# Performance work log

Hardware: AMD Instinct MI355X
Metric: run time of the kernel (lower is better)

The kernel has to match this reference:

```python
import jax, jax.numpy as jnp
import numpy as np

FX, FY, CX, CY = 48.0, 48.0, 48.0, 36.0
H, W = int(2 * CY), int(2 * CX)  # 72, 96
N = H * W  # 6912


def _yz1_grid():
    # K layout as in source: [[cx, fx, 0], [cy, 0, fy], [1, 0, 0]]
    K = np.array([[CX, FX, 0.0], [CY, 0.0, FY], [1.0, 0.0, 0.0]], dtype=np.float64)
    invK = np.linalg.inv(K).astype(np.float32)
    u = np.arange(W, dtype=np.float32)
    v = np.arange(H, dtype=np.float32)
    uu = np.tile(u, H)              # row-major flatten of (H, W) u-grid
    vv = np.repeat(v, W)
    uv1 = np.stack([uu, vv, np.ones_like(uu)], axis=0)  # (3, N)
    return jnp.asarray(invK @ uv1)  # (3, N)


def _kern_mat(p1, p2, dist_coef):
    # p1: (B,3,N1), p2: (B,3,N2) -> exp(-||p1_i - p2_j|| * coef): (B,N1,N2)
    sq1 = jnp.sum(p1 * p1, axis=1)                      # (B,N1)
    sq2 = jnp.sum(p2 * p2, axis=1)                      # (B,N2)
    cross = jnp.einsum('bcn,bcm->bnm', p1, p2)          # (B,N1,N2)
    d2 = jnp.maximum(sq1[:, :, None] + sq2[:, None, :] - 2.0 * cross, 0.0)
    return jnp.exp(-jnp.sqrt(d2) * dist_coef)


def _gramian_feat(f1, f2):
    # norm_mode=1, kernalize=False, L2_norm=True path of gramian()
    B, C = f1.shape[0], f1.shape[1]
    ff1 = f1.reshape(B, C, -1)                          # (B,C,N1)
    ff2 = f2.reshape(B, C, -1)
    n1 = jnp.linalg.norm(ff1, axis=1)                   # (B,N1)
    n2 = jnp.linalg.norm(ff2, axis=1)
    fea_norm_sum = jnp.sum(n1) + jnp.sum(n2)
    ff1 = ff1 / n1[:, None, :]
    ff2 = ff2 / n2[:, None, :]
    gram = jnp.einsum('bcn,bcm->bnm', ff1, ff2)         # (B,N1,N2)
    return gram, fea_norm_sum


def reference(feature1, feature2, depth1, depth2, pose1_2, pose1_2_noise, img1, img2):
    B = depth1.shape[0]
    yz1 = _yz1_grid()                                    # (3,N)
    xyz1 = yz1[None] * depth1.reshape(B, 1, -1)          # (B,3,N)
    xyz2 = yz1[None] * depth2.reshape(B, 1, -1)

    ones = jnp.ones((B, 1, xyz2.shape[2]), dtype=xyz2.dtype)
    xyz2_homo = jnp.concatenate([xyz2, ones], axis=1)    # (B,4,N)
    xyz2_trans = jnp.matmul(pose1_2, xyz2_homo)[:, 0:3, :]

    gram_feat, fea_norm_sum = _gramian_feat(feature1, feature2)
    pcl_diff_exp = _kern_mat(xyz1, xyz2_trans, 0.1)

    fea_norm_sum = fea_norm_sum * 100.0                  # L2_norm & diff_mode

    pose_noisy = jnp.matmul(pose1_2, pose1_2_noise)      # (B,4,4)
    xyz2_trans_noisy = jnp.matmul(pose_noisy, xyz2_homo)[:, 0:3, :]
    pcl_diff_exp_noisy = _kern_mat(xyz1, xyz2_trans_noisy, 0.1)

    inner_neg = -jnp.sum((pcl_diff_exp - pcl_diff_exp_noisy) * gram_feat)
    final_loss = inner_neg                               # sparse_mode=False
    return final_loss, inner_neg, fea_norm_sum


def setup_inputs() -> dict:
    key = jax.random.key(0)
    ks = jax.random.split(key, 8)
    B, C = 1, 16
    feature1 = jax.random.normal(ks[0], (B, C, H, W), dtype=jnp.float32)
    feature2 = jax.random.normal(ks[1], (B, C, H, W), dtype=jnp.float32)
    depth1 = jax.random.uniform(ks[2], (B, 1, H, W), dtype=jnp.float32, minval=0.5, maxval=5.0)
    depth2 = jax.random.uniform(ks[3], (B, 1, H, W), dtype=jnp.float32, minval=0.5, maxval=5.0)
    # pose near identity (rigid-ish transform with small perturbation)
    eye = jnp.eye(4, dtype=jnp.float32)
    dp = 0.05 * jax.random.normal(ks[4], (4, 4), dtype=jnp.float32)
    pose1_2 = (eye + dp.at[3].set(0.0))[None]           # (1,4,4), keep last row [0,0,0,1]
    dn = 0.05 * jax.random.normal(ks[5], (4, 4), dtype=jnp.float32)
    pose1_2_noise = eye + dn.at[3].set(0.0)
    img1 = jax.random.uniform(ks[6], (B, 3, H, W), dtype=jnp.float32)
    img2 = jax.random.uniform(ks[7], (B, 3, H, W), dtype=jnp.float32)
    return {"feature1": feature1, "feature2": feature2, "depth1": depth1,
            "depth2": depth2, "pose1_2": pose1_2, "pose1_2_noise": pose1_2_noise,
            "img1": img1, "img2": img2}
```

## Files before the change

kernel.cpp:

```cpp
#include <hip/hip_runtime.h>
#include <math.h>

#define NPIX 6912
#define IMW  96
#define NJC  64
#define JLEN (NPIX / NJC)

#define OFF_PACK1 0
#define OFF_PACK2 (OFF_PACK1 + NPIX * 4)
#define OFF_F1N   (OFF_PACK2 + NPIX * 8)
#define OFF_F2N   (OFF_F1N + NPIX * 16)

#if __has_builtin(__builtin_amdgcn_exp2f)
#define EXP2F(x) __builtin_amdgcn_exp2f(x)
#else
#define EXP2F(x) exp2f(x)
#endif
#if __has_builtin(__builtin_amdgcn_sqrtf)
#define SQRTF(x) __builtin_amdgcn_sqrtf(x)
#else
#define SQRTF(x) sqrtf(x)
#endif
#define NEG_COEF_LOG2E (-0.14426950408889634f)

__device__ __forceinline__ float blk_reduce256(float v) {
  __shared__ float sm[4];
#pragma unroll
  for (int o = 32; o > 0; o >>= 1) v += __shfl_down(v, o, 64);
  const int lane = threadIdx.x & 63;
  const int wv = threadIdx.x >> 6;
  if (lane == 0) sm[wv] = v;
  __syncthreads();
  return (sm[0] + sm[1]) + (sm[2] + sm[3]);
}

__global__ __launch_bounds__(256) void k_pre(
    const float* __restrict__ f1, const float* __restrict__ f2,
    const float* __restrict__ dep1, const float* __restrict__ dep2,
    const float* __restrict__ pose, const float* __restrict__ noise,
    float* __restrict__ ws, float* __restrict__ out) {
  __shared__ float sPose[24];
  const int t = threadIdx.x;
  if (t < 12) {
    sPose[t] = pose[t];
  } else if (t < 24) {
    const int u = t - 12, r = u >> 2, c = u & 3;
    float s = 0.f;
#pragma unroll
    for (int k = 0; k < 4; ++k) s = fmaf(pose[r * 4 + k], noise[k * 4 + c], s);
    sPose[t] = s;
  }
  __syncthreads();

  const int i = blockIdx.x * 256 + t;
  const int vi = i / IMW;
  const int ui = i - vi * IMW;
  const float inv48 = (float)(1.0 / 48.0);
  const float p1c = fmaf((float)ui, inv48, -1.0f);
  const float p2c = fmaf((float)vi, inv48, -0.75f);

  const float d1 = dep1[i];
  const float x0 = d1, x1 = d1 * p1c, x2 = d1 * p2c;
  const float sq1 = fmaf(x2, x2, fmaf(x1, x1, x0 * x0));
  *(float4*)(ws + OFF_PACK1 + (size_t)i * 4) = make_float4(x0, x1, x2, sq1);

  const float d2 = dep2[i];
  const float w0 = d2, w1 = d2 * p1c, w2 = d2 * p2c;
  const float* P  = sPose;
  const float* Pn = sPose + 12;
  const float y0 = fmaf(P[0], w0, fmaf(P[1], w1, fmaf(P[2],  w2, P[3])));
  const float y1 = fmaf(P[4], w0, fmaf(P[5], w1, fmaf(P[6],  w2, P[7])));
  const float y2 = fmaf(P[8], w0, fmaf(P[9], w1, fmaf(P[10], w2, P[11])));
  const float sq2 = fmaf(y2, y2, fmaf(y1, y1, y0 * y0));
  const float z0 = fmaf(Pn[0], w0, fmaf(Pn[1], w1, fmaf(Pn[2],  w2, Pn[3])));
  const float z1 = fmaf(Pn[4], w0, fmaf(Pn[5], w1, fmaf(Pn[6],  w2, Pn[7])));
  const float z2 = fmaf(Pn[8], w0, fmaf(Pn[9], w1, fmaf(Pn[10], w2, Pn[11])));
  const float sq2n = fmaf(z2, z2, fmaf(z1, z1, z0 * z0));
  *(float4*)(ws + OFF_PACK2 + (size_t)i * 8)     = make_float4(y0, y1, y2, sq2);
  *(float4*)(ws + OFF_PACK2 + (size_t)i * 8 + 4) = make_float4(z0, z1, z2, sq2n);

  float a[16], b[16];
  float sa = 0.f, sb = 0.f;
#pragma unroll
  for (int c = 0; c < 16; ++c) {
    a[c] = f1[c * NPIX + i]; sa = fmaf(a[c], a[c], sa);
    b[c] = f2[c * NPIX + i]; sb = fmaf(b[c], b[c], sb);
  }
  const float na = sqrtf(sa), nb = sqrtf(sb);
#pragma unroll
  for (int c = 0; c < 16; ++c) { a[c] = a[c] / na; b[c] = b[c] / nb; }
#pragma unroll
  for (int c = 0; c < 16; c += 4) {
    *(float4*)(ws + OFF_F1N + (size_t)i * 16 + c) = make_float4(a[c], a[c+1], a[c+2], a[c+3]);
    *(float4*)(ws + OFF_F2N + (size_t)i * 16 + c) = make_float4(b[c], b[c+1], b[c+2], b[c+3]);
  }
  const float part = blk_reduce256(na + nb);
  if (t == 0) atomicAdd(out + 2, 100.0f * part);
}

__global__ __launch_bounds__(256) void k_main(const float* __restrict__ ws,
                                              float* __restrict__ out) {
  __shared__ float4 sF[JLEN * 4];
  __shared__ float4 sP[JLEN * 2];

  const int j0 = blockIdx.y * JLEN;
  const float4* gF = (const float4*)(ws + OFF_F2N)   + (size_t)j0 * 4;
  const float4* gP = (const float4*)(ws + OFF_PACK2) + (size_t)j0 * 2;
  for (int tt = threadIdx.x; tt < JLEN * 4; tt += 256) sF[tt] = gF[tt];
  for (int tt = threadIdx.x; tt < JLEN * 2; tt += 256) sP[tt] = gP[tt];

  const int i = blockIdx.x * 256 + threadIdx.x;
  const float4 pk = *(const float4*)(ws + OFF_PACK1 + (size_t)i * 4);
  const float x0 = pk.x, x1 = pk.y, x2 = pk.z, sq1 = pk.w;
  float f1r[16];
#pragma unroll
  for (int c = 0; c < 16; c += 4) {
    const float4 tq = *(const float4*)(ws + OFF_F1N + (size_t)i * 16 + c);
    f1r[c] = tq.x; f1r[c+1] = tq.y; f1r[c+2] = tq.z; f1r[c+3] = tq.w;
  }
  __syncthreads();

  float acc0 = 0.f, acc1 = 0.f;
#pragma unroll 2
  for (int jj = 0; jj < JLEN; ++jj) {
    const float4 fa = sF[jj * 4 + 0];
    const float4 fb = sF[jj * 4 + 1];
    const float4 fc = sF[jj * 4 + 2];
    const float4 fd = sF[jj * 4 + 3];
    const float4 q  = sP[jj * 2 + 0];
    const float4 r  = sP[jj * 2 + 1];

    float g0 = fmaf(f1r[12], fd.x, fmaf(f1r[8],  fc.x, fmaf(f1r[4], fb.x, f1r[0] * fa.x)));
    float g1 = fmaf(f1r[13], fd.y, fmaf(f1r[9],  fc.y, fmaf(f1r[5], fb.y, f1r[1] * fa.y)));
    float g2 = fmaf(f1r[14], fd.z, fmaf(f1r[10], fc.z, fmaf(f1r[6], fb.z, f1r[2] * fa.z)));
    float g3 = fmaf(f1r[15], fd.w, fmaf(f1r[11], fc.w, fmaf(f1r[7], fb.w, f1r[3] * fa.w)));
    const float g = (g0 + g1) + (g2 + g3);

    const float dt = fmaf(x2, q.z, fmaf(x1, q.y, x0 * q.x));
    float d2 = fmaf(-2.f, dt, sq1 + q.w);
    d2 = fmaxf(d2, 0.f);
    const float k1 = EXP2F(NEG_COEF_LOG2E * SQRTF(d2));
    const float dtn = fmaf(x2, r.z, fmaf(x1, r.y, x0 * r.x));
    float d2n = fmaf(-2.f, dtn, sq1 + r.w);
    d2n = fmaxf(d2n, 0.f);
    const float k2 = EXP2F(NEG_COEF_LOG2E * SQRTF(d2n));

    if (jj & 1) acc1 = fmaf(k1 - k2, g, acc1);
    else        acc0 = fmaf(k1 - k2, g, acc0);
  }
  const float part = blk_reduce256(acc0 + acc1);
  if (threadIdx.x == 0) {
    atomicAdd(out + 0, -part);
    atomicAdd(out + 1, -part);
  }
}

extern "C" void kernel_launch(void* const* d_in, const int* in_sizes, int n_in,
                              void* d_out, int out_size, void* d_ws, size_t ws_size,
                              hipStream_t stream) {
  const float* f1    = (const float*)d_in[0];
  const float* f2    = (const float*)d_in[1];
  const float* dep1  = (const float*)d_in[2];
  const float* dep2  = (const float*)d_in[3];
  const float* pose  = (const float*)d_in[4];
  const float* noise = (const float*)d_in[5];
  float* out = (float*)d_out;
  float* ws  = (float*)d_ws;

  hipMemsetAsync(out, 0, (size_t)out_size * sizeof(float), stream);
  k_pre<<<NPIX / 256, 256, 0, stream>>>(f1, f2, dep1, dep2, pose, noise, ws, out);
  k_main<<<dim3(NPIX / 256, NJC), 256, 0, stream>>>(ws, out);
}
```

Measured before the change: 130.7 us.

## Compute feature gram with fp16 split-precision MFMA and prescale distance constants

Moves the 16-channel feature dot products from scalar FMAs onto MFMA 16x16x32 fp16 instructions. To keep accuracy, each normalized feature is split into high and low fp16 parts, and three of the four cross terms are computed. The distance terms are prescaled by the squared coefficient so the kernel computes exp2(-sqrt(s)) directly. The work is retiled so each wave handles 16 rows against 128-column chunks. This cuts the scalar ALU cost of the gram term, but adds fp16 rounding error and a more complex shared-memory layout.

Measured after the change: 227.1 us. 73.8% more time.

```diff
diff --git a/kernel.cpp b/kernel.cpp
--- a/kernel.cpp
+++ b/kernel.cpp
@@ -3,13 +3,14 @@
 
 #define NPIX 6912
 #define IMW  96
-#define NJC  64
-#define JLEN (NPIX / NJC)
+#define JCH  128
+#define GJ   54
+#define NTILE 8
 
 #define OFF_PACK1 0
-#define OFF_PACK2 (OFF_PACK1 + NPIX * 4)
-#define OFF_F1N   (OFF_PACK2 + NPIX * 8)
-#define OFF_F2N   (OFF_F1N + NPIX * 16)
+#define OFF_PACK2 (NPIX * 4)
+#define OFF_F1P   (NPIX * 12)
+#define OFF_F2P   (NPIX * 28)
 
 #if __has_builtin(__builtin_amdgcn_exp2f)
 #define EXP2F(x) __builtin_amdgcn_exp2f(x)
@@ -22,6 +23,18 @@
 #define SQRTF(x) sqrtf(x)
 #endif
 #define NEG_COEF_LOG2E (-0.14426950408889634f)
+#define CT2   (NEG_COEF_LOG2E * NEG_COEF_LOG2E)
+#define M2CT2 (-2.0f * CT2)
+
+typedef _Float16 f16x8 __attribute__((ext_vector_type(8)));
+typedef float f32x4v __attribute__((ext_vector_type(4)));
+
+__device__ __forceinline__ float packh2(_Float16 a, _Float16 b) {
+  unsigned short ua = __builtin_bit_cast(unsigned short, a);
+  unsigned short ub = __builtin_bit_cast(unsigned short, b);
+  unsigned int u = (unsigned int)ua | ((unsigned int)ub << 16);
+  return __builtin_bit_cast(float, u);
+}
 
 __device__ __forceinline__ float blk_reduce256(float v) {
   __shared__ float sm[4];
@@ -76,8 +89,10 @@
   const float z1 = fmaf(Pn[4], w0, fmaf(Pn[5], w1, fmaf(Pn[6],  w2, Pn[7])));
   const float z2 = fmaf(Pn[8], w0, fmaf(Pn[9], w1, fmaf(Pn[10], w2, Pn[11])));
   const float sq2n = fmaf(z2, z2, fmaf(z1, z1, z0 * z0));
-  *(float4*)(ws + OFF_PACK2 + (size_t)i * 8)     = make_float4(y0, y1, y2, sq2);
-  *(float4*)(ws + OFF_PACK2 + (size_t)i * 8 + 4) = make_float4(z0, z1, z2, sq2n);
+  *(float4*)(ws + OFF_PACK2 + (size_t)i * 8) =
+      make_float4(M2CT2 * y0, M2CT2 * y1, M2CT2 * y2, CT2 * sq2);
+  *(float4*)(ws + OFF_PACK2 + (size_t)i * 8 + 4) =
+      make_float4(M2CT2 * z0, M2CT2 * z1, M2CT2 * z2, CT2 * sq2n);
 
   float a[16], b[16];
   float sa = 0.f, sb = 0.f;
@@ -89,10 +104,27 @@
   const float na = sqrtf(sa), nb = sqrtf(sb);
 #pragma unroll
   for (int c = 0; c < 16; ++c) { a[c] = a[c] / na; b[c] = b[c] / nb; }
-#pragma unroll
-  for (int c = 0; c < 16; c += 4) {
-    *(float4*)(ws + OFF_F1N + (size_t)i * 16 + c) = make_float4(a[c], a[c+1], a[c+2], a[c+3]);
-    *(float4*)(ws + OFF_F2N + (size_t)i * 16 + c) = make_float4(b[c], b[c+1], b[c+2], b[c+3]);
+
+  _Float16 h1v[16], l1v[16], h2v[16], l2v[16];
+#pragma unroll
+  for (int c = 0; c < 16; ++c) {
+    _Float16 h = (_Float16)a[c];
+    h1v[c] = h; l1v[c] = (_Float16)(a[c] - (float)h);
+    _Float16 g = (_Float16)b[c];
+    h2v[c] = g; l2v[c] = (_Float16)(b[c] - (float)g);
+  }
+  float4* p1 = (float4*)(ws + OFF_F1P) + (size_t)i * 4;
+  float4* p2 = (float4*)(ws + OFF_F2P) + (size_t)i * 4;
+#pragma unroll
+  for (int k = 0; k < 2; ++k) {
+    p1[k]     = make_float4(packh2(h1v[k*8+0],h1v[k*8+1]), packh2(h1v[k*8+2],h1v[k*8+3]),
+                            packh2(h1v[k*8+4],h1v[k*8+5]), packh2(h1v[k*8+6],h1v[k*8+7]));
+    p1[k + 2] = make_float4(packh2(l1v[k*8+0],l1v[k*8+1]), packh2(l1v[k*8+2],l1v[k*8+3]),
+                            packh2(l1v[k*8+4],l1v[k*8+5]), packh2(l1v[k*8+6],l1v[k*8+7]));
+    p2[k]     = make_float4(packh2(h2v[k*8+0],h2v[k*8+1]), packh2(h2v[k*8+2],h2v[k*8+3]),
+                            packh2(h2v[k*8+4],h2v[k*8+5]), packh2(h2v[k*8+6],h2v[k*8+7]));
+    p2[k + 2] = make_float4(packh2(l2v[k*8+0],l2v[k*8+1]), packh2(l2v[k*8+2],l2v[k*8+3]),
+                            packh2(l2v[k*8+4],l2v[k*8+5]), packh2(l2v[k*8+6],l2v[k*8+7]));
   }
   const float part = blk_reduce256(na + nb);
   if (t == 0) atomicAdd(out + 2, 100.0f * part);
@@ -100,56 +132,78 @@
 
 __global__ __launch_bounds__(256) void k_main(const float* __restrict__ ws,
                                               float* __restrict__ out) {
-  __shared__ float4 sF[JLEN * 4];
-  __shared__ float4 sP[JLEN * 2];
-
-  const int j0 = blockIdx.y * JLEN;
-  const float4* gF = (const float4*)(ws + OFF_F2N)   + (size_t)j0 * 4;
-  const float4* gP = (const float4*)(ws + OFF_PACK2) + (size_t)j0 * 2;
-  for (int tt = threadIdx.x; tt < JLEN * 4; tt += 256) sF[tt] = gF[tt];
-  for (int tt = threadIdx.x; tt < JLEN * 2; tt += 256) sP[tt] = gP[tt];
-
-  const int i = blockIdx.x * 256 + threadIdx.x;
-  const float4 pk = *(const float4*)(ws + OFF_PACK1 + (size_t)i * 4);
-  const float x0 = pk.x, x1 = pk.y, x2 = pk.z, sq1 = pk.w;
-  float f1r[16];
-#pragma unroll
-  for (int c = 0; c < 16; c += 4) {
-    const float4 tq = *(const float4*)(ws + OFF_F1N + (size_t)i * 16 + c);
-    f1r[c] = tq.x; f1r[c+1] = tq.y; f1r[c+2] = tq.z; f1r[c+3] = tq.w;
-  }
+  __shared__ float4 sB1[NTILE * 64];
+  __shared__ float4 sB2[NTILE * 32];
+  __shared__ float4 sD[NTILE * 16 * 3];
+  __shared__ float4 sZ[1];
+
+  const int t = threadIdx.x;
+  const int j0 = blockIdx.y * JCH;
+  const float4* gF = (const float4*)(ws + OFF_F2P)   + (size_t)j0 * 4;
+  const float4* gD = (const float4*)(ws + OFF_PACK2) + (size_t)j0 * 2;
+
+  for (int idx = t; idx < NTILE * 64; idx += 256) {
+    const int tile = idx >> 6, l = idx & 63;
+    sB1[idx] = gF[(tile * 16 + (l & 15)) * 4 + ((l >> 4) & 1)];
+  }
+  for (int idx = t; idx < NTILE * 32; idx += 256) {
+    const int tile = idx >> 5, l = idx & 31;
+    sB2[idx] = gF[(tile * 16 + (l & 15)) * 4 + 2 + (l >> 4)];
+  }
+  for (int idx = t; idx < NTILE * 16 * 2; idx += 256) {
+    const int row = idx >> 1, half = idx & 1;
+    sD[row * 3 + half] = gD[row * 2 + half];
+  }
+  if (t == 0) sZ[0] = make_float4(0.f, 0.f, 0.f, 0.f);
+
+  const int wid = t >> 6, lane = t & 63;
+  const int c = lane & 15, g = lane >> 4;
+  const int rowbase = (blockIdx.x * 4 + wid) * 16;
+
+  const f16x8 afrag = *(const f16x8*)((const char*)(ws + OFF_F1P)
+                                      + (size_t)(rowbase + c) * 64 + g * 16);
+  float4 xr[4];
+#pragma unroll
+  for (int p = 0; p < 4; ++p) {
+    xr[p] = *(const float4*)(ws + OFF_PACK1 + (size_t)(rowbase + g * 4 + p) * 4);
+    xr[p].w *= CT2;
+  }
+
   __syncthreads();
 
-  float acc0 = 0.f, acc1 = 0.f;
-#pragma unroll 2
-  for (int jj = 0; jj < JLEN; ++jj) {
-    const float4 fa = sF[jj * 4 + 0];
-    const float4 fb = sF[jj * 4 + 1];
-    const float4 fc = sF[jj * 4 + 2];
-    const float4 fd = sF[jj * 4 + 3];
-    const float4 q  = sP[jj * 2 + 0];
-    const float4 r  = sP[jj * 2 + 1];
-
-    float g0 = fmaf(f1r[12], fd.x, fmaf(f1r[8],  fc.x, fmaf(f1r[4], fb.x, f1r[0] * fa.x)));
-    float g1 = fmaf(f1r[13], fd.y, fmaf(f1r[9],  fc.y, fmaf(f1r[5], fb.y, f1r[1] * fa.y)));
-    float g2 = fmaf(f1r[14], fd.z, fmaf(f1r[10], fc.z, fmaf(f1r[6], fb.z, f1r[2] * fa.z)));
-    float g3 = fmaf(f1r[15], fd.w, fmaf(f1r[11], fc.w, fmaf(f1r[7], fb.w, f1r[3] * fa.w)));
-    const float g = (g0 + g1) + (g2 + g3);
-
-    const float dt = fmaf(x2, q.z, fmaf(x1, q.y, x0 * q.x));
-    float d2 = fmaf(-2.f, dt, sq1 + q.w);
-    d2 = fmaxf(d2, 0.f);
-    const float k1 = EXP2F(NEG_COEF_LOG2E * SQRTF(d2));
-    const float dtn = fmaf(x2, r.z, fmaf(x1, r.y, x0 * r.x));
-    float d2n = fmaf(-2.f, dtn, sq1 + r.w);
-    d2n = fmaxf(d2n, 0.f);
-    const float k2 = EXP2F(NEG_COEF_LOG2E * SQRTF(d2n));
-
-    if (jj & 1) acc1 = fmaf(k1 - k2, g, acc1);
-    else        acc0 = fmaf(k1 - k2, g, acc0);
-  }
-  const float part = blk_reduce256(acc0 + acc1);
-  if (threadIdx.x == 0) {
+  const float4* pb2 = (lane < 32) ? (sB2 + lane) : sZ;
+  const int st2 = (lane < 32) ? 32 : 0;
+
+  float accv = 0.f;
+  for (int jt = 0; jt < NTILE; ++jt) {
+    const f16x8 b1 = *(const f16x8*)(sB1 + jt * 64 + lane);
+    const f16x8 b2 = *(const f16x8*)(pb2 + jt * st2);
+    f32x4v acc = {0.f, 0.f, 0.f, 0.f};
+    acc = __builtin_amdgcn_mfma_f32_16x16x32_f16(afrag, b1, acc, 0, 0, 0);
+    acc = __builtin_amdgcn_mfma_f32_16x16x32_f16(afrag, b2, acc, 0, 0, 0);
+
+    const float4 q = sD[(jt * 16 + c) * 3];
+    const float4 r = sD[(jt * 16 + c) * 3 + 1];
+#pragma unroll
+    for (int p = 0; p < 4; ++p) {
+      const float4 X = xr[p];
+      float s1 = X.w + q.w;
+      s1 = fmaf(X.x, q.x, s1);
+      s1 = fmaf(X.y, q.y, s1);
+      s1 = fmaf(X.z, q.z, s1);
+      s1 = fmaxf(s1, 0.f);
+      const float k1 = EXP2F(-SQRTF(s1));
+      float s2 = X.w + r.w;
+      s2 = fmaf(X.x, r.x, s2);
+      s2 = fmaf(X.y, r.y, s2);
+      s2 = fmaf(X.z, r.z, s2);
+      s2 = fmaxf(s2, 0.f);
+      const float k2 = EXP2F(-SQRTF(s2));
+      accv = fmaf(k1 - k2, acc[p], accv);
+    }
+  }
+  const float part = blk_reduce256(accv);
+  if (t == 0) {
     atomicAdd(out + 0, -part);
     atomicAdd(out + 1, -part);
   }
@@ -167,7 +221,7 @@
   float* out = (float*)d_out;
   float* ws  = (float*)d_ws;
 
-  hipMemsetAsync(out, 0, (size_t)out_size * sizeof(float), stream);
+  (void)hipMemsetAsync(out, 0, (size_t)out_size * sizeof(float), stream);
   k_pre<<<NPIX / 256, 256, 0, stream>>>(f1, f2, dep1, dep2, pose, noise, ws, out);
-  k_main<<<dim3(NPIX / 256, NJC), 256, 0, stream>>>(ws, out);
-}
+  k_main<<<dim3(NPIX / (4 * 16), GJ), 256, 0, stream>>>(ws, out);
+}
```
